# Performance work log

Hardware: AMD Instinct MI355X
Metric: run time of the kernel (lower is better)

## Reference

```python
import jax, jax.numpy as jnp
import numpy as np

B, N, D = 256, 196, 1024   # batch, regions, vis_embed_dim
HID, ATT, SIN, WID, ISD = 1024, 256, 1024, 1024, 256
S = 10                      # sentence steps


def _lin(key, out_dim, in_dim):
    kw, kb = jax.random.split(key)
    w = jax.random.normal(kw, (out_dim, in_dim), jnp.float32) * 0.02
    b = jax.random.normal(kb, (out_dim,), jnp.float32) * 0.02
    return w, b


def setup_inputs() -> dict:
    key = jax.random.key(0)
    ks = jax.random.split(key, 16)
    inp = {}
    inp['vis_enc'] = jax.random.normal(ks[0], (B, N, D), jnp.float32)
    inp['sentences'] = jax.random.randint(ks[1], (B, S, 50), 0, 10000, jnp.int64)
    inp['enc_att_w'], inp['enc_att_b'] = _lin(ks[2], ATT, D)
    inp['dec_att_w'], inp['dec_att_b'] = _lin(ks[3], ATT, HID)
    inp['full_att_w'], inp['full_att_b'] = _lin(ks[4], 1, ATT)
    inp['ctx_w'], inp['ctx_b'] = _lin(ks[5], SIN, D)
    inp['W_ih'], inp['b_ih'] = _lin(ks[6], 4 * HID, SIN)
    inp['W_hh'], inp['b_hh'] = _lin(ks[7], 4 * HID, HID)
    inp['topic_hid_w'], inp['topic_hid_b'] = _lin(ks[8], WID, HID)
    inp['topic_ctx_w'], inp['topic_ctx_b'] = _lin(ks[9], WID, SIN)
    inp['stop_prev_w'], inp['stop_prev_b'] = _lin(ks[10], ISD, HID)
    inp['stop_cur_w'], inp['stop_cur_b'] = _lin(ks[11], ISD, HID)
    inp['final_stop_w'], inp['final_stop_b'] = _lin(ks[12], 2, ISD)
    return inp


def reference(vis_enc, sentences,
              enc_att_w, enc_att_b, dec_att_w, dec_att_b, full_att_w, full_att_b,
              ctx_w, ctx_b, W_ih, b_ih, W_hh, b_hh,
              topic_hid_w, topic_hid_b, topic_ctx_w, topic_ctx_b,
              stop_prev_w, stop_prev_b, stop_cur_w, stop_cur_b,
              final_stop_w, final_stop_b):
    batch, hid = vis_enc.shape[0], W_hh.shape[1]
    sent_num = sentences.shape[1]
    # encoder projection is h-independent -> hoist out of the recurrence
    vis_enc_att = jnp.einsum('bnd,ad->bna', vis_enc, enc_att_w) + enc_att_b  # [B,N,ATT]

    def step(carry, _):
        h, c = carry
        # CoAtt additive attention
        dec = h @ dec_att_w.T + dec_att_b                       # [B,ATT]
        join = jnp.tanh(vis_enc_att + dec[:, None, :])          # [B,N,ATT]
        logits = jnp.einsum('bna,a->bn', join, full_att_w[0]) + full_att_b[0]
        scores = jax.nn.softmax(logits, axis=1)                 # [B,N]
        att_out = jnp.einsum('bn,bnd->bd', scores, vis_enc)     # [B,D]
        ctx = att_out @ ctx_w.T + ctx_b                         # [B,SIN]
        h_prev = h
        # LSTMCell
        gates = ctx @ W_ih.T + b_ih + h @ W_hh.T + b_hh         # [B,4H]
        i, f, g, o = jnp.split(gates, 4, axis=1)
        c_new = jax.nn.sigmoid(f) * c + jax.nn.sigmoid(i) * jnp.tanh(g)
        h_new = jax.nn.sigmoid(o) * jnp.tanh(c_new)
        # topic + stop heads
        topic = jnp.tanh(h_new @ topic_hid_w.T + topic_hid_b
                         + ctx @ topic_ctx_w.T + topic_ctx_b)   # [B,WID]
        p = jnp.tanh(h_prev @ stop_prev_w.T + stop_prev_b
                     + h_new @ stop_cur_w.T + stop_cur_b)
        p = p @ final_stop_w.T + final_stop_b                   # [B,2]
        return (h_new, c_new), (topic, p)

    h0 = jnp.zeros((batch, hid), vis_enc.dtype)
    c0 = jnp.zeros((batch, hid), vis_enc.dtype)
    _, (topics, ps) = jax.lax.scan(step, (h0, c0), None, length=sent_num)
    topics = jnp.transpose(topics, (1, 0, 2))  # [B,S,WID]
    ps = jnp.transpose(ps, (1, 0, 2))          # [B,S,2]
    return topics, ps
```

## Files before the change

kernel.cpp:

```cpp
#include <hip/hip_runtime.h>
#include <hip/hip_bf16.h>
#include <math.h>

static constexpr int BB = 256;
static constexpr int NR = 196;
static constexpr int DV = 1024;
static constexpr int HH = 1024;
static constexpr int AT = 256;
static constexpr int SI = 1024;
static constexpr int WI = 1024;
static constexpr int IS = 256;
static constexpr int ST = 10;

__device__ __forceinline__ float sigmoidf_(float x) { return 1.0f / (1.0f + expf(-x)); }

__device__ __forceinline__ ushort f2bf(float x) {
    uint u = __float_as_uint(x);
    return (ushort)((u + 0x7FFFu + ((u >> 16) & 1u)) >> 16);
}
__device__ __forceinline__ float bf2f(ushort b) { return __uint_as_float(((uint)b) << 16); }

using bf16x8 = __attribute__((ext_vector_type(8))) short;
using f32x4  = __attribute__((ext_vector_type(4))) float;
#define MFMA_B16(a, b, c) __builtin_amdgcn_mfma_f32_16x16x32_bf16((a), (b), (c), 0, 0, 0)

struct CvtTab { const float* s[8]; ushort* h[8]; ushort* l[8]; };

__global__ __launch_bounds__(256) void setup_all(
    CvtTab tab,
    const float* __restrict__ ctxw, ushort* __restrict__ ctT_h, ushort* __restrict__ ctT_l,
    const float* __restrict__ Wih, const float* __restrict__ Wtc,
    const float* __restrict__ cb,
    const float* __restrict__ bih, const float* __restrict__ btc,
    float* __restrict__ out_ih, float* __restrict__ out_tc,
    const float* __restrict__ vis_src, ushort* __restrict__ vis_dst)
{
    __shared__ float T[32][33];
    const int bid = blockIdx.x;

    if (bid < 11264) {
        const int cum[9] = {0, 256, 4352, 5376, 5632, 5888, 6144, 10240, 11264};
        int seg = 0;
#pragma unroll
        for (int i = 1; i < 8; ++i) if (bid >= cum[i]) seg = i;
        const float* s = tab.s[seg];
        ushort* h = tab.h[seg];
        ushort* l = tab.l[seg];
        const int r = bid - cum[seg];
        int rd = r;
        if (seg == 1) rd = (r & 1023) * 4 + (r >> 10);
        const int src = r * 1024 + threadIdx.x * 4;
        const size_t dst = (size_t)rd * 1024 + threadIdx.x * 4;
        float4 v = *(const float4*)(s + src);
        ushort h0 = f2bf(v.x), h1 = f2bf(v.y), h2 = f2bf(v.z), h3 = f2bf(v.w);
        uint2 hq;
        hq.x = h0 | ((uint)h1 << 16); hq.y = h2 | ((uint)h3 << 16);
        *(uint2*)(h + dst) = hq;
        if (seg != 5) {
            uint2 lq;
            ushort l0 = f2bf(v.x - bf2f(h0)), l1 = f2bf(v.y - bf2f(h1));
            ushort l2 = f2bf(v.z - bf2f(h2)), l3 = f2bf(v.w - bf2f(h3));
            lq.x = l0 | ((uint)l1 << 16); lq.y = l2 | ((uint)l3 << 16);
            *(uint2*)(l + dst) = lq;
        }
    } else if (bid < 12288) {
        const int lb = bid - 11264;
        const int tx = threadIdx.x & 31, ty = threadIdx.x >> 5;
        const int k0 = (lb & 31) * 32, n0 = (lb >> 5) * 32;
#pragma unroll
        for (int j = 0; j < 4; ++j)
            T[ty + 8 * j][tx] = ctxw[(size_t)(k0 + ty + 8 * j) * 1024 + n0 + tx];
        __syncthreads();
#pragma unroll
        for (int j = 0; j < 4; ++j) {
            const float v = T[tx][ty + 8 * j];
            const ushort h = f2bf(v);
            const size_t o = (size_t)(n0 + ty + 8 * j) * 1024 + k0 + tx;
            ctT_h[o] = h;
            ctT_l[o] = f2bf(v - bf2f(h));
        }
    } else if (bid < 13568) {
        const int lb = bid - 12288;
        const int lane = threadIdx.x & 63;
        const float* W; const float* b; float* out; int n;
        if (lb < 1024) { W = Wih; b = bih; out = out_ih; n = lb * 4 + (threadIdx.x >> 6); }
        else { W = Wtc; b = btc; out = out_tc; n = (lb - 1024) * 4 + (threadIdx.x >> 6); }
        const float* wr = W + (size_t)n * 1024;
        float p = 0.f;
#pragma unroll
        for (int i = 0; i < 4; ++i) {
            const float4 wv = *(const float4*)&wr[i * 256 + lane * 4];
            const float4 vv = *(const float4*)&cb[i * 256 + lane * 4];
            p = fmaf(wv.x, vv.x, p); p = fmaf(wv.y, vv.y, p);
            p = fmaf(wv.z, vv.z, p); p = fmaf(wv.w, vv.w, p);
        }
        for (int off = 32; off; off >>= 1) p += __shfl_down(p, off);
        if (lane == 0) out[n] = p + b[n];
    } else {
        const int lb = bid - 13568;
        const size_t i = ((size_t)lb * 256 + threadIdx.x) * 8;
        const float4 v0 = *(const float4*)(vis_src + i);
        const float4 v1 = *(const float4*)(vis_src + i + 4);
        uint4 o;
        o.x = f2bf(v0.x) | ((uint)f2bf(v0.y) << 16);
        o.y = f2bf(v0.z) | ((uint)f2bf(v0.w) << 16);
        o.z = f2bf(v1.x) | ((uint)f2bf(v1.y) << 16);
        o.w = f2bf(v1.z) | ((uint)f2bf(v1.w) << 16);
        *(uint4*)(vis_dst + i) = o;
    }
}

__global__ __launch_bounds__(256) void mgemm_wsp2(
    const ushort* __restrict__ A1h, const ushort* __restrict__ A1l,
    ushort* __restrict__ C1h, ushort* __restrict__ C1l,
    const ushort* __restrict__ A2h, const ushort* __restrict__ A2l,
    ushort* __restrict__ C2h, ushort* __restrict__ C2l,
    const ushort* __restrict__ Wh, const ushort* __restrict__ Wl)
{
    __shared__ __align__(16) ushort SM[4 * 64 * 40];
    ushort* Ah = SM; ushort* Al = SM + 2560; ushort* Bh = SM + 5120; ushort* Bl = SM + 7680;

    const int bid = blockIdx.x;
    const int seg1 = (bid < 1024) ? 1 : 0;
    const int lb = seg1 ? bid : (bid - 1024);
    const int bx = lb & 15, by = lb >> 4;
    const int m0 = by * 64, n0 = bx * 64;
    const ushort* Ahg = seg1 ? A1h : A2h;
    const ushort* Alg = seg1 ? A1l : A2l;
    ushort* Ch = seg1 ? C1h : C2h;
    ushort* Cl = seg1 ? C1l : C2l;
    const int N = SI, K = DV;

    const int t = threadIdx.x;
    const int w = t >> 6, lane = t & 63;
    const int l15 = lane & 15, q = lane >> 4;
    const int sr = t >> 2, sq = (t & 3) * 8;
    const int nch = K >> 5;

    f32x4 acc[4] = {};
    uint4 pah, pal, pbh, pbl;
    auto pref = [&](int c) {
        const int k0 = c << 5;
        const size_t ab = (size_t)(m0 + sr) * K + k0 + sq;
        pah = *(const uint4*)&Ahg[ab];
        pal = *(const uint4*)&Alg[ab];
        pbh = *(const uint4*)&Wh[(size_t)(n0 + sr) * K + k0 + sq];
        pbl = *(const uint4*)&Wl[(size_t)(n0 + sr) * K + k0 + sq];
    };
    pref(0);

    for (int c = 0; c < nch; ++c) {
        __syncthreads();
        *(uint4*)&Ah[sr * 40 + sq] = pah;
        *(uint4*)&Al[sr * 40 + sq] = pal;
        *(uint4*)&Bh[sr * 40 + sq] = pbh;
        *(uint4*)&Bl[sr * 40 + sq] = pbl;
        __syncthreads();
        if (c + 1 < nch) pref(c + 1);
        const bf16x8 bh = *(const bf16x8*)&Bh[(w * 16 + l15) * 40 + q * 8];
        const bf16x8 bl = *(const bf16x8*)&Bl[(w * 16 + l15) * 40 + q * 8];
#pragma unroll
        for (int mi = 0; mi < 4; ++mi) {
            const bf16x8 ah = *(const bf16x8*)&Ah[(mi * 16 + l15) * 40 + q * 8];
            const bf16x8 al = *(const bf16x8*)&Al[(mi * 16 + l15) * 40 + q * 8];
            acc[mi] = MFMA_B16(ah, bh, acc[mi]);
            acc[mi] = MFMA_B16(ah, bl, acc[mi]);
            acc[mi] = MFMA_B16(al, bh, acc[mi]);
        }
    }

    const int col = n0 + w * 16 + l15;
#pragma unroll
    for (int mi = 0; mi < 4; ++mi) {
#pragma unroll
        for (int j = 0; j < 4; ++j) {
            const int row = m0 + mi * 16 + q * 4 + j;
            const int ro = seg1 ? ((row & 1023) * 4 + (row >> 10)) : row;
            const float v = acc[mi][j];
            const ushort h = f2bf(v);
            Ch[(size_t)ro * N + col] = h;
            Cl[(size_t)ro * N + col] = f2bf(v - bf2f(h));
        }
    }
}

__global__ __launch_bounds__(256) void mgemm_heads(
    const ushort* __restrict__ tA1h, const ushort* __restrict__ tA1l,
    const ushort* __restrict__ tW1h, const ushort* __restrict__ tW1l,
    const float* __restrict__ tb1,
    const ushort* __restrict__ tA2h, const ushort* __restrict__ tA2l,
    const ushort* __restrict__ tW2h, const ushort* __restrict__ tW2l,
    const float* __restrict__ tb2,
    float* __restrict__ tC,
    const ushort* __restrict__ sA1h, const ushort* __restrict__ sA1l,
    const ushort* __restrict__ sW1h, const ushort* __restrict__ sW1l,
    const float* __restrict__ sb1,
    const ushort* __restrict__ sA2h, const ushort* __restrict__ sA2l,
    const ushort* __restrict__ sW2h, const ushort* __restrict__ sW2l,
    const float* __restrict__ sb2,
    float* __restrict__ sC)
{
    __shared__ __align__(16) ushort SM[4 * 64 * 40];
    ushort* Ah = SM; ushort* Al = SM + 2560; ushort* Bh = SM + 5120; ushort* Bl = SM + 7680;

    const int bid = blockIdx.x;
    const int topic = (bid < 640) ? 1 : 0;
    const int lb = topic ? bid : (bid - 640);
    const int bx = topic ? (lb & 15) : (lb & 3);
    const int by = topic ? (lb >> 4) : (lb >> 2);
    const int m0 = by * 64, n0 = bx * 64;
    const int ldc = topic ? WI : IS;

    const ushort* A1h = topic ? tA1h : sA1h;  const ushort* A1l = topic ? tA1l : sA1l;
    const ushort* W1h = topic ? tW1h : sW1h;  const ushort* W1l = topic ? tW1l : sW1l;
    const float*  b1  = topic ? tb1  : sb1;
    const ushort* A2h = topic ? tA2h : sA2h;  const ushort* A2l = topic ? tA2l : sA2l;
    const ushort* W2h = topic ? tW2h : sW2h;  const ushort* W2l = topic ? tW2l : sW2l;
    const float*  b2  = topic ? tb2  : sb2;
    float* C = topic ? tC : sC;

    const int t = threadIdx.x;
    const int w = t >> 6, lane = t & 63;
    const int l15 = lane & 15, q = lane >> 4;
    const int sr = t >> 2, sq = (t & 3) * 8;
    const int K = HH;
    const int KC = K >> 5, nch = 2 * KC;

    f32x4 acc[4] = {};
    uint4 pah, pal, pbh, pbl;

    auto pref = [&](int c) {
        const int pass = (c >= KC) ? 1 : 0;
        const int k0 = (c - pass * KC) << 5;
        const ushort* Axh = pass ? A2h : A1h;
        const ushort* Axl = pass ? A2l : A1l;
        const ushort* Wh = pass ? W2h : W1h;
        const ushort* Wl = pass ? W2l : W1l;
        const size_t ab = (size_t)(m0 + sr) * K + k0 + sq;
        pah = *(const uint4*)&Axh[ab];
        pal = *(const uint4*)&Axl[ab];
        pbh = *(const uint4*)&Wh[(size_t)(n0 + sr) * K + k0 + sq];
        pbl = *(const uint4*)&Wl[(size_t)(n0 + sr) * K + k0 + sq];
    };
    pref(0);

    for (int c = 0; c < nch; ++c) {
        __syncthreads();
        *(uint4*)&Ah[sr * 40 + sq] = pah;
        *(uint4*)&Al[sr * 40 + sq] = pal;
        *(uint4*)&Bh[sr * 40 + sq] = pbh;
        *(uint4*)&Bl[sr * 40 + sq] = pbl;
        __syncthreads();
        if (c + 1 < nch) pref(c + 1);
        const bf16x8 bh = *(const bf16x8*)&Bh[(w * 16 + l15) * 40 + q * 8];
        const bf16x8 bl = *(const bf16x8*)&Bl[(w * 16 + l15) * 40 + q * 8];
#pragma unroll
        for (int mi = 0; mi < 4; ++mi) {
            const bf16x8 ah = *(const bf16x8*)&Ah[(mi * 16 + l15) * 40 + q * 8];
            const bf16x8 al = *(const bf16x8*)&Al[(mi * 16 + l15) * 40 + q * 8];
            acc[mi] = MFMA_B16(ah, bh, acc[mi]);
            acc[mi] = MFMA_B16(ah, bl, acc[mi]);
            acc[mi] = MFMA_B16(al, bh, acc[mi]);
        }
    }

    const int col = n0 + w * 16 + l15;
    const float bias = b1[col] + b2[col];
#pragma unroll
    for (int mi = 0; mi < 4; ++mi) {
#pragma unroll
        for (int j = 0; j < 4; ++j) {
            const int row = m0 + mi * 16 + q * 4 + j;
            const float v = tanhf(acc[mi][j] + bias);
            if (topic)
                C[((size_t)(row & 255) * ST + (row >> 8)) * ldc + col] = v;
            else
                C[(size_t)row * ldc + col] = v;
        }
    }
}

__global__ __launch_bounds__(512, 6) void mgemm8_lstm(
    const ushort* __restrict__ A1h, const ushort* __restrict__ A1l,
    const ushort* __restrict__ W1h, const ushort* __restrict__ W1l,
    const float* __restrict__ b1,
    const ushort* __restrict__ A2h, const ushort* __restrict__ A2l,
    const ushort* __restrict__ W2h, const ushort* __restrict__ W2l,
    const float* __restrict__ b2,
    int K, float* __restrict__ cvec,
    ushort* __restrict__ hnh, ushort* __restrict__ hnl)
{
    __shared__ __align__(16) ushort SM[26624];

    const int t = threadIdx.x;
    const int m0 = blockIdx.y * 64, n0 = blockIdx.x * 32;
    const int w = t >> 6, lane = t & 63;
    const int g = w >> 2, wg = w & 3;
    const int l15 = lane & 15, q = lane >> 4;
    const int tl = t & 255;
    const int sr = tl >> 2, sq4 = (tl & 3) * 16;
    const int br = tl >> 3, bq = (tl & 7) * 8;
    const int mh = wg >> 1;
    const int colL = (wg & 1) * 16 + l15;

    ushort* Ah = SM + g * 13312;
    ushort* Al = Ah + 4608;
    ushort* Bh = Al + 4608;
    ushort* Bl = Bh + 2048;

    const int nchg = K >> 6;
    const ushort* Ahg = g ? A2h : A1h;
    const ushort* Alg = g ? A2l : A1l;
    const ushort* Wh  = g ? W2h : W1h;
    const ushort* Wl  = g ? W2l : W1l;

    const int bwi = br * 64 + (bq ^ ((br & 7) << 3));

    f32x4 acc[2] = {};
    uint4 pah0, pah1, pal0, pal1, pbh, pbl;
    auto pref = [&](int c) {
        const int k0 = c << 6;
        const size_t ab = (size_t)(m0 + sr) * K + k0 + sq4;
        pah0 = *(const uint4*)&Ahg[ab];
        pah1 = *(const uint4*)&Ahg[ab + 8];
        pal0 = *(const uint4*)&Alg[ab];
        pal1 = *(const uint4*)&Alg[ab + 8];
        pbh = *(const uint4*)&Wh[(size_t)(n0 + br) * K + k0 + bq];
        pbl = *(const uint4*)&Wl[(size_t)(n0 + br) * K + k0 + bq];
    };
    pref(0);

    for (int c = 0; c < nchg; ++c) {
        __syncthreads();
        *(uint4*)&Ah[sr * 72 + sq4]     = pah0;
        *(uint4*)&Ah[sr * 72 + sq4 + 8] = pah1;
        *(uint4*)&Al[sr * 72 + sq4]     = pal0;
        *(uint4*)&Al[sr * 72 + sq4 + 8] = pal1;
        *(uint4*)&Bh[bwi] = pbh;
        *(uint4*)&Bl[bwi] = pbl;
        __syncthreads();
        if (c + 1 < nchg) pref(c + 1);
#pragma unroll
        for (int ks = 0; ks < 2; ++ks) {
            const int bro = colL * 64 + ((ks * 32 + q * 8) ^ ((colL & 7) << 3));
            const bf16x8 bh = *(const bf16x8*)&Bh[bro];
            const bf16x8 bl = *(const bf16x8*)&Bl[bro];
#pragma unroll
            for (int i = 0; i < 2; ++i) {
                const int mi = mh * 2 + i;
                const bf16x8 ah = *(const bf16x8*)&Ah[(mi * 16 + l15) * 72 + ks * 32 + q * 8];
                const bf16x8 al = *(const bf16x8*)&Al[(mi * 16 + l15) * 72 + ks * 32 + q * 8];
                acc[i] = MFMA_B16(ah, bh, acc[i]);
                acc[i] = MFMA_B16(ah, bl, acc[i]);
                acc[i] = MFMA_B16(al, bh, acc[i]);
            }
        }
    }

    float* comb = (float*)(SM + 13312);
    __syncthreads();
    if (g == 1) {
#pragma unroll
        for (int i = 0; i < 2; ++i)
#pragma unroll
            for (int j = 0; j < 4; ++j) comb[tl * 9 + i * 4 + j] = acc[i][j];
    }
    __syncthreads();
    if (g == 0) {
#pragma unroll
        for (int i = 0; i < 2; ++i)
#pragma unroll
            for (int j = 0; j < 4; ++j) acc[i][j] += comb[tl * 9 + i * 4 + j];
    }

    float* G = (float*)(SM + 17920);
    if (g == 0) {
        const int colG = n0 + colL;
        const int gate = colG & 3, unit = colG >> 2;
        const float bias = b1[gate * 1024 + unit] + b2[gate * 1024 + unit];
#pragma unroll
        for (int i = 0; i < 2; ++i) {
            const int mi = mh * 2 + i;
#pragma unroll
            for (int j = 0; j < 4; ++j)
                G[(mi * 16 + q * 4 + j) * 40 + colL] = acc[i][j] + bias;
        }
    }
    __syncthreads();
    {
        const int row = t >> 3, ul = t & 7;
        const float4 g4 = *(const float4*)&G[row * 40 + ul * 4];
        const size_t ci = (size_t)(m0 + row) * HH + (n0 >> 2) + ul;
        const float cn = sigmoidf_(g4.y) * cvec[ci] + sigmoidf_(g4.x) * tanhf(g4.z);
        cvec[ci] = cn;
        const float hv = sigmoidf_(g4.w) * tanhf(cn);
        const ushort hhi = f2bf(hv);
        hnh[ci] = hhi;
        hnl[ci] = f2bf(hv - bf2f(hhi));
    }
}

__global__ __launch_bounds__(512) void mgemm_preb(
    const ushort* __restrict__ vh, const ushort* __restrict__ Wh, const ushort* __restrict__ Wl,
    const float* __restrict__ bias, ushort* __restrict__ C)
{
    __shared__ __align__(16) ushort Avh[128 * 40];
    __shared__ __align__(16) ushort Bh[256 * 40];
    __shared__ __align__(16) ushort Bl[256 * 40];

    const int t = threadIdx.x;
    const int m0 = blockIdx.x * 128;
    const int w = t >> 6, lane = t & 63;
    const int rg = w >> 2, cg = w & 3;
    const int l15 = lane & 15, q = lane >> 4;
    const int ar = t >> 2, ac = (t & 3) * 8;
    const int brr = t >> 1, bc = (t & 1) * 16;
    const int K = DV;

    f32x4 acc[4][4] = {};
    uint4 pa, pbh0, pbh1, pbl0, pbl1;
    auto pref = [&](int c) {
        const int k0 = c << 5;
        pa   = *(const uint4*)&vh[(size_t)(m0 + ar) * K + k0 + ac];
        const size_t bb = (size_t)brr * K + k0 + bc;
        pbh0 = *(const uint4*)&Wh[bb];
        pbh1 = *(const uint4*)&Wh[bb + 8];
        pbl0 = *(const uint4*)&Wl[bb];
        pbl1 = *(const uint4*)&Wl[bb + 8];
    };
    pref(0);

    for (int c = 0; c < 32; ++c) {
        __syncthreads();
        *(uint4*)&Avh[ar * 40 + ac] = pa;
        *(uint4*)&Bh[brr * 40 + bc]     = pbh0;
        *(uint4*)&Bh[brr * 40 + bc + 8] = pbh1;
        *(uint4*)&Bl[brr * 40 + bc]     = pbl0;
        *(uint4*)&Bl[brr * 40 + bc + 8] = pbl1;
        __syncthreads();
        if (c + 1 < 32) pref(c + 1);

        bf16x8 ah[4];
#pragma unroll
        for (int mi = 0; mi < 4; ++mi)
            ah[mi] = *(const bf16x8*)&Avh[(rg * 64 + mi * 16 + l15) * 40 + q * 8];
#pragma unroll
        for (int ni = 0; ni < 4; ++ni) {
            const bf16x8 bh = *(const bf16x8*)&Bh[(cg * 64 + ni * 16 + l15) * 40 + q * 8];
            const bf16x8 bl = *(const bf16x8*)&Bl[(cg * 64 + ni * 16 + l15) * 40 + q * 8];
#pragma unroll
            for (int mi = 0; mi < 4; ++mi) {
                acc[mi][ni] = MFMA_B16(ah[mi], bh, acc[mi][ni]);
                acc[mi][ni] = MFMA_B16(ah[mi], bl, acc[mi][ni]);
            }
        }
    }

#pragma unroll
    for (int ni = 0; ni < 4; ++ni) {
        const int col = cg * 64 + ni * 16 + l15;
        const float bb = bias[col];
#pragma unroll
        for (int mi = 0; mi < 4; ++mi)
#pragma unroll
            for (int j = 0; j < 4; ++j) {
                const int row = m0 + rg * 64 + mi * 16 + q * 4 + j;
                C[(size_t)row * AT + col] = f2bf(acc[mi][ni][j] + bb);
            }
    }
}

template <int VBF>
__global__ __launch_bounds__(1024) void att_step(
    const ushort* __restrict__ vis_att,
    const ushort* __restrict__ hch, const ushort* __restrict__ hcl,
    const ushort* __restrict__ dec_wh, const float* __restrict__ dec_b,
    const float* __restrict__ fw, const float* __restrict__ fbp,
    const void* __restrict__ visp,
    ushort* __restrict__ att_h, ushort* __restrict__ att_l)
{
    const int b = blockIdx.x;
    const int t = threadIdx.x;
    const int lane = t & 63;
    const int w = t >> 6;

    __shared__ float hs[HH];
    __shared__ float decs[AT];
    __shared__ float fwv[AT];
    __shared__ float logit[NR + 4];
    __shared__ float sc[NR + 4];
    __shared__ float red[8];
    __shared__ float part[8][DV];

    hs[t] = bf2f(hch[(size_t)b * HH + t]) + bf2f(hcl[(size_t)b * HH + t]);
    if (t < AT) fwv[t] = fw[t];
    __syncthreads();
    const float fb = fbp[0];

#pragma unroll
    for (int j = 0; j < 16; ++j) {
        const int a = w * 16 + j;
        const ushort* wr = dec_wh + (size_t)a * HH;
        float p = 0.f;
#pragma unroll
        for (int i = 0; i < 2; ++i) {
            const uint4 wv = *(const uint4*)&wr[i * 512 + lane * 8];
            const float4 hv0 = *(const float4*)&hs[i * 512 + lane * 8];
            const float4 hv1 = *(const float4*)&hs[i * 512 + lane * 8 + 4];
            p = fmaf(bf2f((ushort)(wv.x & 0xFFFF)), hv0.x, p);
            p = fmaf(bf2f((ushort)(wv.x >> 16)),    hv0.y, p);
            p = fmaf(bf2f((ushort)(wv.y & 0xFFFF)), hv0.z, p);
            p = fmaf(bf2f((ushort)(wv.y >> 16)),    hv0.w, p);
            p = fmaf(bf2f((ushort)(wv.z & 0xFFFF)), hv1.x, p);
            p = fmaf(bf2f((ushort)(wv.z >> 16)),    hv1.y, p);
            p = fmaf(bf2f((ushort)(wv.w & 0xFFFF)), hv1.z, p);
            p = fmaf(bf2f((ushort)(wv.w >> 16)),    hv1.w, p);
        }
        for (int off = 32; off; off >>= 1) p += __shfl_down(p, off);
        if (lane == 0) decs[a] = p + dec_b[a];
    }
    __syncthreads();

    for (int n = w; n < NR; n += 16) {
        const ushort4 v4 = *(const ushort4*)&vis_att[((size_t)b * NR + n) * AT + lane * 4];
        const int a = lane * 4;
        float s = tanhf(bf2f(v4.x) + decs[a]) * fwv[a];
        s = fmaf(tanhf(bf2f(v4.y) + decs[a + 1]), fwv[a + 1], s);
        s = fmaf(tanhf(bf2f(v4.z) + decs[a + 2]), fwv[a + 2], s);
        s = fmaf(tanhf(bf2f(v4.w) + decs[a + 3]), fwv[a + 3], s);
        for (int off = 32; off; off >>= 1) s += __shfl_down(s, off);
        if (lane == 0) logit[n] = s + fb;
    }
    __syncthreads();

    float m = -1e30f, e = 0.f;
    if (t < NR) m = logit[t];
    if (t < 256) {
        for (int off = 32; off; off >>= 1) m = fmaxf(m, __shfl_down(m, off));
        if (lane == 0) red[w] = m;
    }
    __syncthreads();
    m = fmaxf(fmaxf(red[0], red[1]), fmaxf(red[2], red[3]));
    if (t < NR) e = expf(logit[t] - m);
    if (t < 256) {
        float ss = e;
        for (int off = 32; off; off >>= 1) ss += __shfl_down(ss, off);
        if (lane == 0) red[4 + w] = ss;
    }
    __syncthreads();
    const float S = red[4] + red[5] + red[6] + red[7];
    if (t < NR) sc[t] = e / S;
    __syncthreads();

    const int slice = t >> 7;
    const int c8 = (t & 127) * 8;
    const int nbeg = (slice <= 4) ? 25 * slice : 100 + 24 * (slice - 4);
    const int nend = (slice < 4) ? nbeg + 25 : nbeg + 24;
    float a0 = 0.f, a1 = 0.f, a2 = 0.f, a3 = 0.f;
    float a4 = 0.f, a5 = 0.f, a6 = 0.f, a7 = 0.f;
    if (VBF) {
        const ushort* vb = (const ushort*)visp + (size_t)b * NR * DV + c8;
        for (int n = nbeg; n < nend; ++n) {
            const float s = sc[n];
            const uint4 v = *(const uint4*)&vb[(size_t)n * DV];
            a0 = fmaf(s, bf2f((ushort)(v.x & 0xFFFF)), a0);
            a1 = fmaf(s, bf2f((ushort)(v.x >> 16)), a1);
            a2 = fmaf(s, bf2f((ushort)(v.y & 0xFFFF)), a2);
            a3 = fmaf(s, bf2f((ushort)(v.y >> 16)), a3);
            a4 = fmaf(s, bf2f((ushort)(v.z & 0xFFFF)), a4);
            a5 = fmaf(s, bf2f((ushort)(v.z >> 16)), a5);
            a6 = fmaf(s, bf2f((ushort)(v.w & 0xFFFF)), a6);
            a7 = fmaf(s, bf2f((ushort)(v.w >> 16)), a7);
        }
    } else {
        const float* vb = (const float*)visp + (size_t)b * NR * DV + c8;
        for (int n = nbeg; n < nend; ++n) {
            const float s = sc[n];
            const float4 v0 = *(const float4*)&vb[(size_t)n * DV];
            const float4 v1 = *(const float4*)&vb[(size_t)n * DV + 4];
            a0 = fmaf(s, v0.x, a0); a1 = fmaf(s, v0.y, a1);
            a2 = fmaf(s, v0.z, a2); a3 = fmaf(s, v0.w, a3);
            a4 = fmaf(s, v1.x, a4); a5 = fmaf(s, v1.y, a5);
            a6 = fmaf(s, v1.z, a6); a7 = fmaf(s, v1.w, a7);
        }
    }
    float4 av0; av0.x = a0; av0.y = a1; av0.z = a2; av0.w = a3;
    float4 av1; av1.x = a4; av1.y = a5; av1.z = a6; av1.w = a7;
    *(float4*)&part[slice][c8]     = av0;
    *(float4*)&part[slice][c8 + 4] = av1;
    __syncthreads();
    const float v = ((part[0][t] + part[1][t]) + (part[2][t] + part[3][t]))
                  + ((part[4][t] + part[5][t]) + (part[6][t] + part[7][t]));
    const ushort vh16 = f2bf(v);
    att_h[(size_t)b * DV + t] = vh16;
    att_l[(size_t)b * DV + t] = f2bf(v - bf2f(vh16));
}

__global__ __launch_bounds__(256) void stop_final_all(
    const float* __restrict__ pt, const float* __restrict__ fw,
    const float* __restrict__ fb, float* __restrict__ outp)
{
    const int row = blockIdx.x;
    const int s = row >> 8, b = row & 255;
    const int t = threadIdx.x;
    const int lane = t & 63;
    const int w = t >> 6;

    __shared__ float red[16];
    const float v = pt[(size_t)row * IS + t];
    float p0 = v * fw[t];
    float p1 = v * fw[IS + t];
    for (int off = 32; off; off >>= 1) {
        p0 += __shfl_down(p0, off);
        p1 += __shfl_down(p1, off);
    }
    if (lane == 0) { red[w] = p0; red[8 + w] = p1; }
    __syncthreads();
    if (t == 0) {
        outp[((size_t)b * ST + s) * 2 + 0] = red[0] + red[1] + red[2] + red[3] + fb[0];
        outp[((size_t)b * ST + s) * 2 + 1] = red[8] + red[9] + red[10] + red[11] + fb[1];
    }
}

extern "C" void kernel_launch(void* const* d_in, const int* in_sizes, int n_in,
                              void* d_out, int out_size, void* d_ws, size_t ws_size,
                              hipStream_t stream)
{
    const float* vis        = (const float*)d_in[0];
    const float* enc_att_w  = (const float*)d_in[2];
    const float* enc_att_b  = (const float*)d_in[3];
    const float* dec_att_w  = (const float*)d_in[4];
    const float* dec_att_b  = (const float*)d_in[5];
    const float* full_att_w = (const float*)d_in[6];
    const float* full_att_b = (const float*)d_in[7];
    const float* ctx_w      = (const float*)d_in[8];
    const float* ctx_b      = (const float*)d_in[9];
    const float* W_ih       = (const float*)d_in[10];
    const float* b_ih       = (const float*)d_in[11];
    const float* W_hh       = (const float*)d_in[12];
    const float* b_hh       = (const float*)d_in[13];
    const float* topic_hid_w = (const float*)d_in[14];
    const float* topic_hid_b = (const float*)d_in[15];
    const float* topic_ctx_w = (const float*)d_in[16];
    const float* topic_ctx_b = (const float*)d_in[17];
    const float* stop_prev_w = (const float*)d_in[18];
    const float* stop_prev_b = (const float*)d_in[19];
    const float* stop_cur_w  = (const float*)d_in[20];
    const float* stop_cur_b  = (const float*)d_in[21];
    const float* final_stop_w = (const float*)d_in[22];
    const float* final_stop_b = (const float*)d_in[23];

    float* out_topics = (float*)d_out;
    float* out_ps     = (float*)d_out + (size_t)BB * ST * WI;

    char* ws = (char*)d_ws;
    size_t off = 0;
    auto alloc = [&](size_t bytes) -> void* {
        void* p = (void*)(ws + off);
        off += (bytes + 255) & ~(size_t)255;
        return p;
    };
    ushort* vis_att = (ushort*)alloc((size_t)BB * NR * AT * 2);
    const size_t WTOT = (size_t)11264 * 1024;
    ushort* wh = (ushort*)alloc(WTOT * 2);
    ushort* wl = (ushort*)alloc(WTOT * 2);
    ushort* hh_h   = (ushort*)alloc((size_t)(ST + 1) * BB * HH * 2);
    ushort* hh_l   = (ushort*)alloc((size_t)(ST + 1) * BB * HH * 2);
    ushort* att_all_h = (ushort*)alloc((size_t)ST * BB * DV * 2);
    ushort* att_all_l = (ushort*)alloc((size_t)ST * BB * DV * 2);
    float* cbuf    = (float*)alloc((size_t)BB * HH * 4);
    float* pt_all  = (float*)alloc((size_t)ST * BB * IS * 4);
    ushort* ctT_h  = (ushort*)alloc((size_t)SI * DV * 2);
    ushort* ctT_l  = (ushort*)alloc((size_t)SI * DV * 2);
    ushort* cmb_h  = (ushort*)alloc((size_t)4 * HH * SI * 2);
    ushort* cmb_l  = (ushort*)alloc((size_t)4 * HH * SI * 2);
    ushort* tcc_h  = (ushort*)alloc((size_t)WI * SI * 2);
    ushort* tcc_l  = (ushort*)alloc((size_t)WI * SI * 2);
    float* bf_ih   = (float*)alloc((size_t)4 * HH * 4);
    float* bf_tc   = (float*)alloc((size_t)WI * 4);
    if (off > ws_size) return;
    ushort* vis_bf = nullptr;
    {
        const size_t need = (size_t)BB * NR * DV * 2;
        if (off + need <= ws_size) vis_bf = (ushort*)alloc(need);
    }

    const size_t O_ENC = 0;
    const size_t O_HH  = 262144;
    const size_t O_TH  = 4456448;
    const size_t O_SP  = 5505024;
    const size_t O_SC  = 5767168;
    const size_t O_DEC = 6029312;
    const size_t O_IH2 = 6291456;
    const size_t O_TC2 = 10485760;

    CvtTab tab;
    const float* srcs[8] = {enc_att_w, W_hh, topic_hid_w, stop_prev_w, stop_cur_w,
                            dec_att_w, W_ih, topic_ctx_w};
    const size_t offs[8] = {O_ENC, O_HH, O_TH, O_SP, O_SC, O_DEC, O_IH2, O_TC2};
    for (int i = 0; i < 8; ++i) {
        tab.s[i] = srcs[i];
        tab.h[i] = wh + offs[i];
        tab.l[i] = wl + offs[i];
    }

    hipMemsetAsync(hh_h, 0, (size_t)BB * HH * 2, stream);
    hipMemsetAsync(hh_l, 0, (size_t)BB * HH * 2, stream);
    hipMemsetAsync(cbuf, 0, (size_t)BB * HH * 4, stream);

    setup_all<<<38656, 256, 0, stream>>>(
        tab, ctx_w, ctT_h, ctT_l,
        W_ih, topic_ctx_w, ctx_b, b_ih, topic_ctx_b, bf_ih, bf_tc,
        vis, vis_bf);

    mgemm_wsp2<<<1280, 256, 0, stream>>>(
        wh + O_IH2, wl + O_IH2, cmb_h, cmb_l,
        wh + O_TC2, wl + O_TC2, tcc_h, tcc_l,
        ctT_h, ctT_l);

    mgemm_preb<<<(BB * NR) / 128, 512, 0, stream>>>(
        vis_bf, wh + O_ENC, wl + O_ENC, enc_att_b, vis_att);

    for (int s = 0; s < ST; ++s) {
        ushort* hch = hh_h + (size_t)s * BB * HH;
        ushort* hcl = hh_l + (size_t)s * BB * HH;
        ushort* hnh = hh_h + (size_t)(s + 1) * BB * HH;
        ushort* hnl = hh_l + (size_t)(s + 1) * BB * HH;
        ushort* ath = att_all_h + (size_t)s * BB * DV;
        ushort* atl = att_all_l + (size_t)s * BB * DV;
        att_step<1><<<BB, 1024, 0, stream>>>(vis_att, hch, hcl, wh + O_DEC, dec_att_b,
                                             full_att_w, full_att_b, vis_bf,
                                             ath, atl);
        mgemm8_lstm<<<dim3(4 * HH / 32, BB / 64), 512, 0, stream>>>(
            ath, atl, cmb_h, cmb_l, bf_ih,
            hch, hcl, wh + O_HH, wl + O_HH, b_hh,
            SI, cbuf, hnh, hnl);
    }

    mgemm_heads<<<800, 256, 0, stream>>>(
        hh_h + (size_t)BB * HH, hh_l + (size_t)BB * HH,
        wh + O_TH, wl + O_TH, topic_hid_b,
        att_all_h, att_all_l, tcc_h, tcc_l, bf_tc,
        out_topics,
        hh_h, hh_l, wh + O_SP, wl + O_SP, stop_prev_b,
        hh_h + (size_t)BB * HH, hh_l + (size_t)BB * HH,
        wh + O_SC, wl + O_SC, stop_cur_b,
        pt_all);
    stop_final_all<<<ST * BB, 256, 0, stream>>>(pt_all, final_stop_w, final_stop_b, out_ps);
}
```

Measured before the change: 955.0 us.

## Overlap h@W_hh GEMM with attention step via extra blocks in attention kernel

Moves the recurrent h@W_hh gate GEMM out of the LSTM kernel into 64 extra blocks appended to the attention kernel launch, where it runs concurrently with the per-batch attention blocks and writes fp32 partial gates to a new workspace buffer. The LSTM kernel then splits its K dimension across its two warp groups for the ctx@W_ih product only and adds the precomputed gate partials in the epilogue. This shortens the serial critical path of each recurrent step but adds an extra fp32 gate buffer round trip through memory. The attention kernel now also declares a large static shared array, which may lower its occupancy.

```diff
diff --git a/kernel.cpp b/kernel.cpp
--- a/kernel.cpp
+++ b/kernel.cpp
@@ -280,217 +280,88 @@
     }
 }
 
-__global__ __launch_bounds__(512, 6) void mgemm8_lstm(
-    const ushort* __restrict__ A1h, const ushort* __restrict__ A1l,
-    const ushort* __restrict__ W1h, const ushort* __restrict__ W1l,
-    const float* __restrict__ b1,
-    const ushort* __restrict__ A2h, const ushort* __restrict__ A2l,
-    const ushort* __restrict__ W2h, const ushort* __restrict__ W2l,
-    const float* __restrict__ b2,
-    int K, float* __restrict__ cvec,
-    ushort* __restrict__ hnh, ushort* __restrict__ hnl)
-{
-    __shared__ __align__(16) ushort SM[26624];
-
-    const int t = threadIdx.x;
-    const int m0 = blockIdx.y * 64, n0 = blockIdx.x * 32;
-    const int w = t >> 6, lane = t & 63;
-    const int g = w >> 2, wg = w & 3;
-    const int l15 = lane & 15, q = lane >> 4;
-    const int tl = t & 255;
-    const int sr = tl >> 2, sq4 = (tl & 3) * 16;
-    const int br = tl >> 3, bq = (tl & 7) * 8;
-    const int mh = wg >> 1;
-    const int colL = (wg & 1) * 16 + l15;
-
-    ushort* Ah = SM + g * 13312;
-    ushort* Al = Ah + 4608;
-    ushort* Bh = Al + 4608;
-    ushort* Bl = Bh + 2048;
-
-    const int nchg = K >> 6;
-    const ushort* Ahg = g ? A2h : A1h;
-    const ushort* Alg = g ? A2l : A1l;
-    const ushort* Wh  = g ? W2h : W1h;
-    const ushort* Wl  = g ? W2l : W1l;
-
-    const int bwi = br * 64 + (bq ^ ((br & 7) << 3));
-
-    f32x4 acc[2] = {};
-    uint4 pah0, pah1, pal0, pal1, pbh, pbl;
-    auto pref = [&](int c) {
-        const int k0 = c << 6;
-        const size_t ab = (size_t)(m0 + sr) * K + k0 + sq4;
-        pah0 = *(const uint4*)&Ahg[ab];
-        pah1 = *(const uint4*)&Ahg[ab + 8];
-        pal0 = *(const uint4*)&Alg[ab];
-        pal1 = *(const uint4*)&Alg[ab + 8];
-        pbh = *(const uint4*)&Wh[(size_t)(n0 + br) * K + k0 + bq];
-        pbl = *(const uint4*)&Wl[(size_t)(n0 + br) * K + k0 + bq];
-    };
-    pref(0);
-
-    for (int c = 0; c < nchg; ++c) {
-        __syncthreads();
-        *(uint4*)&Ah[sr * 72 + sq4]     = pah0;
-        *(uint4*)&Ah[sr * 72 + sq4 + 8] = pah1;
-        *(uint4*)&Al[sr * 72 + sq4]     = pal0;
-        *(uint4*)&Al[sr * 72 + sq4 + 8] = pal1;
-        *(uint4*)&Bh[bwi] = pbh;
-        *(uint4*)&Bl[bwi] = pbl;
-        __syncthreads();
-        if (c + 1 < nchg) pref(c + 1);
-#pragma unroll
-        for (int ks = 0; ks < 2; ++ks) {
-            const int bro = colL * 64 + ((ks * 32 + q * 8) ^ ((colL & 7) << 3));
-            const bf16x8 bh = *(const bf16x8*)&Bh[bro];
-            const bf16x8 bl = *(const bf16x8*)&Bl[bro];
-#pragma unroll
-            for (int i = 0; i < 2; ++i) {
-                const int mi = mh * 2 + i;
-                const bf16x8 ah = *(const bf16x8*)&Ah[(mi * 16 + l15) * 72 + ks * 32 + q * 8];
-                const bf16x8 al = *(const bf16x8*)&Al[(mi * 16 + l15) * 72 + ks * 32 + q * 8];
-                acc[i] = MFMA_B16(ah, bh, acc[i]);
-                acc[i] = MFMA_B16(ah, bl, acc[i]);
-                acc[i] = MFMA_B16(al, bh, acc[i]);
-            }
-        }
-    }
-
-    float* comb = (float*)(SM + 13312);
-    __syncthreads();
-    if (g == 1) {
-#pragma unroll
-        for (int i = 0; i < 2; ++i)
-#pragma unroll
-            for (int j = 0; j < 4; ++j) comb[tl * 9 + i * 4 + j] = acc[i][j];
-    }
-    __syncthreads();
-    if (g == 0) {
-#pragma unroll
-        for (int i = 0; i < 2; ++i)
-#pragma unroll
-            for (int j = 0; j < 4; ++j) acc[i][j] += comb[tl * 9 + i * 4 + j];
-    }
-
-    float* G = (float*)(SM + 17920);
-    if (g == 0) {
-        const int colG = n0 + colL;
-        const int gate = colG & 3, unit = colG >> 2;
-        const float bias = b1[gate * 1024 + unit] + b2[gate * 1024 + unit];
-#pragma unroll
-        for (int i = 0; i < 2; ++i) {
-            const int mi = mh * 2 + i;
-#pragma unroll
-            for (int j = 0; j < 4; ++j)
-                G[(mi * 16 + q * 4 + j) * 40 + colL] = acc[i][j] + bias;
-        }
-    }
-    __syncthreads();
-    {
-        const int row = t >> 3, ul = t & 7;
-        const float4 g4 = *(const float4*)&G[row * 40 + ul * 4];
-        const size_t ci = (size_t)(m0 + row) * HH + (n0 >> 2) + ul;
-        const float cn = sigmoidf_(g4.y) * cvec[ci] + sigmoidf_(g4.x) * tanhf(g4.z);
-        cvec[ci] = cn;
-        const float hv = sigmoidf_(g4.w) * tanhf(cn);
-        const ushort hhi = f2bf(hv);
-        hnh[ci] = hhi;
-        hnl[ci] = f2bf(hv - bf2f(hhi));
-    }
-}
-
-__global__ __launch_bounds__(512) void mgemm_preb(
-    const ushort* __restrict__ vh, const ushort* __restrict__ Wh, const ushort* __restrict__ Wl,
-    const float* __restrict__ bias, ushort* __restrict__ C)
-{
-    __shared__ __align__(16) ushort Avh[128 * 40];
-    __shared__ __align__(16) ushort Bh[256 * 40];
-    __shared__ __align__(16) ushort Bl[256 * 40];
-
-    const int t = threadIdx.x;
-    const int m0 = blockIdx.x * 128;
-    const int w = t >> 6, lane = t & 63;
-    const int rg = w >> 2, cg = w & 3;
-    const int l15 = lane & 15, q = lane >> 4;
-    const int ar = t >> 2, ac = (t & 3) * 8;
-    const int brr = t >> 1, bc = (t & 1) * 16;
-    const int K = DV;
-
-    f32x4 acc[4][4] = {};
-    uint4 pa, pbh0, pbh1, pbl0, pbl1;
-    auto pref = [&](int c) {
-        const int k0 = c << 5;
-        pa   = *(const uint4*)&vh[(size_t)(m0 + ar) * K + k0 + ac];
-        const size_t bb = (size_t)brr * K + k0 + bc;
-        pbh0 = *(const uint4*)&Wh[bb];
-        pbh1 = *(const uint4*)&Wh[bb + 8];
-        pbl0 = *(const uint4*)&Wl[bb];
-        pbl1 = *(const uint4*)&Wl[bb + 8];
-    };
-    pref(0);
-
-    for (int c = 0; c < 32; ++c) {
-        __syncthreads();
-        *(uint4*)&Avh[ar * 40 + ac] = pa;
-        *(uint4*)&Bh[brr * 40 + bc]     = pbh0;
-        *(uint4*)&Bh[brr * 40 + bc + 8] = pbh1;
-        *(uint4*)&Bl[brr * 40 + bc]     = pbl0;
-        *(uint4*)&Bl[brr * 40 + bc + 8] = pbl1;
-        __syncthreads();
-        if (c + 1 < 32) pref(c + 1);
-
-        bf16x8 ah[4];
-#pragma unroll
-        for (int mi = 0; mi < 4; ++mi)
-            ah[mi] = *(const bf16x8*)&Avh[(rg * 64 + mi * 16 + l15) * 40 + q * 8];
-#pragma unroll
-        for (int ni = 0; ni < 4; ++ni) {
-            const bf16x8 bh = *(const bf16x8*)&Bh[(cg * 64 + ni * 16 + l15) * 40 + q * 8];
-            const bf16x8 bl = *(const bf16x8*)&Bl[(cg * 64 + ni * 16 + l15) * 40 + q * 8];
-#pragma unroll
-            for (int mi = 0; mi < 4; ++mi) {
-                acc[mi][ni] = MFMA_B16(ah[mi], bh, acc[mi][ni]);
-                acc[mi][ni] = MFMA_B16(ah[mi], bl, acc[mi][ni]);
-            }
-        }
-    }
-
-#pragma unroll
-    for (int ni = 0; ni < 4; ++ni) {
-        const int col = cg * 64 + ni * 16 + l15;
-        const float bb = bias[col];
-#pragma unroll
-        for (int mi = 0; mi < 4; ++mi)
-#pragma unroll
-            for (int j = 0; j < 4; ++j) {
-                const int row = m0 + rg * 64 + mi * 16 + q * 4 + j;
-                C[(size_t)row * AT + col] = f2bf(acc[mi][ni][j] + bb);
-            }
-    }
-}
-
 template <int VBF>
-__global__ __launch_bounds__(1024) void att_step(
+__global__ __launch_bounds__(1024) void att_hgemm(
     const ushort* __restrict__ vis_att,
     const ushort* __restrict__ hch, const ushort* __restrict__ hcl,
     const ushort* __restrict__ dec_wh, const float* __restrict__ dec_b,
     const float* __restrict__ fw, const float* __restrict__ fbp,
     const void* __restrict__ visp,
-    ushort* __restrict__ att_h, ushort* __restrict__ att_l)
+    ushort* __restrict__ att_h, ushort* __restrict__ att_l,
+    const ushort* __restrict__ Whh_h, const ushort* __restrict__ Whh_l,
+    float* __restrict__ Gh)
 {
-    const int b = blockIdx.x;
+    __shared__ __align__(16) char SMRAW[81920];
+    const int bidx = blockIdx.x;
+
+    if (bidx >= BB) {
+        const int lb = bidx - BB;
+        const int sub = threadIdx.x >> 8;
+        const int t = threadIdx.x & 255;
+        ushort* SM = (ushort*)(SMRAW + sub * 20480);
+        ushort* Ah = SM; ushort* Al = SM + 2560;
+        ushort* Bh = SM + 5120; ushort* Bl = SM + 7680;
+        const int tile = lb * 4 + sub;
+        const int m0 = (tile & 3) * 64;
+        const int n0 = (tile >> 2) * 64;
+        const int w = t >> 6, lane = t & 63;
+        const int l15 = lane & 15, q = lane >> 4;
+        const int sr = t >> 2, sq = (t & 3) * 8;
+        const int K = HH, nch = K >> 5;
+
+        f32x4 acc[4] = {};
+        uint4 pah, pal, pbh, pbl;
+        auto pref = [&](int c) {
+            const int k0 = c << 5;
+            const size_t ab = (size_t)(m0 + sr) * K + k0 + sq;
+            pah = *(const uint4*)&hch[ab];
+            pal = *(const uint4*)&hcl[ab];
+            pbh = *(const uint4*)&Whh_h[(size_t)(n0 + sr) * K + k0 + sq];
+            pbl = *(const uint4*)&Whh_l[(size_t)(n0 + sr) * K + k0 + sq];
+        };
+        pref(0);
+
+        for (int c = 0; c < nch; ++c) {
+            __syncthreads();
+            *(uint4*)&Ah[sr * 40 + sq] = pah;
+            *(uint4*)&Al[sr * 40 + sq] = pal;
+            *(uint4*)&Bh[sr * 40 + sq] = pbh;
+            *(uint4*)&Bl[sr * 40 + sq] = pbl;
+            __syncthreads();
+            if (c + 1 < nch) pref(c + 1);
+            const bf16x8 bh = *(const bf16x8*)&Bh[(w * 16 + l15) * 40 + q * 8];
+            const bf16x8 bl = *(const bf16x8*)&Bl[(w * 16 + l15) * 40 + q * 8];
+#pragma unroll
+            for (int mi = 0; mi < 4; ++mi) {
+                const bf16x8 ah = *(const bf16x8*)&Ah[(mi * 16 + l15) * 40 + q * 8];
+                const bf16x8 al = *(const bf16x8*)&Al[(mi * 16 + l15) * 40 + q * 8];
+                acc[mi] = MFMA_B16(ah, bh, acc[mi]);
+                acc[mi] = MFMA_B16(ah, bl, acc[mi]);
+                acc[mi] = MFMA_B16(al, bh, acc[mi]);
+            }
+        }
+
+        const int col = n0 + w * 16 + l15;
+#pragma unroll
+        for (int mi = 0; mi < 4; ++mi)
+#pragma unroll
+            for (int j = 0; j < 4; ++j)
+                Gh[(size_t)(m0 + mi * 16 + q * 4 + j) * 4096 + col] = acc[mi][j];
+        return;
+    }
+
+    float* hs    = (float*)SMRAW;
+    float* decs  = (float*)(SMRAW + 4096);
+    float* fwv   = (float*)(SMRAW + 5120);
+    float* logit = (float*)(SMRAW + 6144);
+    float* sc    = (float*)(SMRAW + 7168);
+    float* red   = (float*)(SMRAW + 8192);
+    float (*part)[DV] = (float(*)[DV])(SMRAW + 8448);
+
+    const int b = bidx;
     const int t = threadIdx.x;
     const int lane = t & 63;
     const int w = t >> 6;
-
-    __shared__ float hs[HH];
-    __shared__ float decs[AT];
-    __shared__ float fwv[AT];
-    __shared__ float logit[NR + 4];
-    __shared__ float sc[NR + 4];
-    __shared__ float red[8];
-    __shared__ float part[8][DV];
 
     hs[t] = bf2f(hch[(size_t)b * HH + t]) + bf2f(hcl[(size_t)b * HH + t]);
     if (t < AT) fwv[t] = fw[t];
@@ -594,6 +465,193 @@
     const ushort vh16 = f2bf(v);
     att_h[(size_t)b * DV + t] = vh16;
     att_l[(size_t)b * DV + t] = f2bf(v - bf2f(vh16));
+}
+
+__global__ __launch_bounds__(512, 6) void mgemm8_lstm(
+    const ushort* __restrict__ A1h, const ushort* __restrict__ A1l,
+    const ushort* __restrict__ W1h, const ushort* __restrict__ W1l,
+    const float* __restrict__ b1, const float* __restrict__ b2,
+    const float* __restrict__ Gh,
+    int K, float* __restrict__ cvec,
+    ushort* __restrict__ hnh, ushort* __restrict__ hnl)
+{
+    __shared__ __align__(16) ushort SM[26624];
+
+    const int t = threadIdx.x;
+    const int m0 = blockIdx.y * 64, n0 = blockIdx.x * 32;
+    const int w = t >> 6, lane = t & 63;
+    const int g = w >> 2, wg = w & 3;
+    const int l15 = lane & 15, q = lane >> 4;
+    const int tl = t & 255;
+    const int sr = tl >> 2, sq4 = (tl & 3) * 16;
+    const int br = tl >> 3, bq = (tl & 7) * 8;
+    const int mh = wg >> 1;
+    const int colL = (wg & 1) * 16 + l15;
+
+    ushort* Ah = SM + g * 13312;
+    ushort* Al = Ah + 4608;
+    ushort* Bh = Al + 4608;
+    ushort* Bl = Bh + 2048;
+
+    const int nchg = K >> 7;
+
+    const int bwi = br * 64 + (bq ^ ((br & 7) << 3));
+
+    f32x4 acc[2] = {};
+    uint4 pah0, pah1, pal0, pal1, pbh, pbl;
+    auto pref = [&](int c) {
+        const int k0 = (c << 6) + (g << 9);
+        const size_t ab = (size_t)(m0 + sr) * K + k0 + sq4;
+        pah0 = *(const uint4*)&A1h[ab];
+        pah1 = *(const uint4*)&A1h[ab + 8];
+        pal0 = *(const uint4*)&A1l[ab];
+        pal1 = *(const uint4*)&A1l[ab + 8];
+        pbh = *(const uint4*)&W1h[(size_t)(n0 + br) * K + k0 + bq];
+        pbl = *(const uint4*)&W1l[(size_t)(n0 + br) * K + k0 + bq];
+    };
+    pref(0);
+
+    for (int c = 0; c < nchg; ++c) {
+        __syncthreads();
+        *(uint4*)&Ah[sr * 72 + sq4]     = pah0;
+        *(uint4*)&Ah[sr * 72 + sq4 + 8] = pah1;
+        *(uint4*)&Al[sr * 72 + sq4]     = pal0;
+        *(uint4*)&Al[sr * 72 + sq4 + 8] = pal1;
+        *(uint4*)&Bh[bwi] = pbh;
+        *(uint4*)&Bl[bwi] = pbl;
+        __syncthreads();
+        if (c + 1 < nchg) pref(c + 1);
+#pragma unroll
+        for (int ks = 0; ks < 2; ++ks) {
+            const int bro = colL * 64 + ((ks * 32 + q * 8) ^ ((colL & 7) << 3));
+            const bf16x8 bh = *(const bf16x8*)&Bh[bro];
+            const bf16x8 bl = *(const bf16x8*)&Bl[bro];
+#pragma unroll
+            for (int i = 0; i < 2; ++i) {
+                const int mi = mh * 2 + i;
+                const bf16x8 ah = *(const bf16x8*)&Ah[(mi * 16 + l15) * 72 + ks * 32 + q * 8];
+                const bf16x8 al = *(const bf16x8*)&Al[(mi * 16 + l15) * 72 + ks * 32 + q * 8];
+                acc[i] = MFMA_B16(ah, bh, acc[i]);
+                acc[i] = MFMA_B16(ah, bl, acc[i]);
+                acc[i] = MFMA_B16(al, bh, acc[i]);
+            }
+        }
+    }
+
+    float* comb = (float*)(SM + 13312);
+    __syncthreads();
+    if (g == 1) {
+#pragma unroll
+        for (int i = 0; i < 2; ++i)
+#pragma unroll
+            for (int j = 0; j < 4; ++j) comb[tl * 9 + i * 4 + j] = acc[i][j];
+    }
+    __syncthreads();
+    if (g == 0) {
+#pragma unroll
+        for (int i = 0; i < 2; ++i)
+#pragma unroll
+            for (int j = 0; j < 4; ++j) acc[i][j] += comb[tl * 9 + i * 4 + j];
+    }
+
+    float* G = (float*)(SM + 17920);
+    if (g == 0) {
+        const int colG = n0 + colL;
+        const int gate = colG & 3, unit = colG >> 2;
+        const float bias = b1[gate * 1024 + unit] + b2[gate * 1024 + unit];
+#pragma unroll
+        for (int i = 0; i < 2; ++i) {
+            const int mi = mh * 2 + i;
+#pragma unroll
+            for (int j = 0; j < 4; ++j) {
+                const int row = mi * 16 + q * 4 + j;
+                G[row * 40 + colL] = acc[i][j] + bias
+                    + Gh[(size_t)(m0 + row) * 4096 + colG];
+            }
+        }
+    }
+    __syncthreads();
+    {
+        const int row = t >> 3, ul = t & 7;
+        const float4 g4 = *(const float4*)&G[row * 40 + ul * 4];
+        const size_t ci = (size_t)(m0 + row) * HH + (n0 >> 2) + ul;
+        const float cn = sigmoidf_(g4.y) * cvec[ci] + sigmoidf_(g4.x) * tanhf(g4.z);
+        cvec[ci] = cn;
+        const float hv = sigmoidf_(g4.w) * tanhf(cn);
+        const ushort hhi = f2bf(hv);
+        hnh[ci] = hhi;
+        hnl[ci] = f2bf(hv - bf2f(hhi));
+    }
+}
+
+__global__ __launch_bounds__(512) void mgemm_preb(
+    const ushort* __restrict__ vh, const ushort* __restrict__ Wh, const ushort* __restrict__ Wl,
+    const float* __restrict__ bias, ushort* __restrict__ C)
+{
+    __shared__ __align__(16) ushort Avh[128 * 40];
+    __shared__ __align__(16) ushort Bh[256 * 40];
+    __shared__ __align__(16) ushort Bl[256 * 40];
+
+    const int t = threadIdx.x;
+    const int m0 = blockIdx.x * 128;
+    const int w = t >> 6, lane = t & 63;
+    const int rg = w >> 2, cg = w & 3;
+    const int l15 = lane & 15, q = lane >> 4;
+    const int ar = t >> 2, ac = (t & 3) * 8;
+    const int brr = t >> 1, bc = (t & 1) * 16;
+    const int K = DV;
+
+    f32x4 acc[4][4] = {};
+    uint4 pa, pbh0, pbh1, pbl0, pbl1;
+    auto pref = [&](int c) {
+        const int k0 = c << 5;
+        pa   = *(const uint4*)&vh[(size_t)(m0 + ar) * K + k0 + ac];
+        const size_t bb = (size_t)brr * K + k0 + bc;
+        pbh0 = *(const uint4*)&Wh[bb];
+        pbh1 = *(const uint4*)&Wh[bb + 8];
+        pbl0 = *(const uint4*)&Wl[bb];
+        pbl1 = *(const uint4*)&Wl[bb + 8];
+    };
+    pref(0);
+
+    for (int c = 0; c < 32; ++c) {
+        __syncthreads();
+        *(uint4*)&Avh[ar * 40 + ac] = pa;
+        *(uint4*)&Bh[brr * 40 + bc]     = pbh0;
+        *(uint4*)&Bh[brr * 40 + bc + 8] = pbh1;
+        *(uint4*)&Bl[brr * 40 + bc]     = pbl0;
+        *(uint4*)&Bl[brr * 40 + bc + 8] = pbl1;
+        __syncthreads();
+        if (c + 1 < 32) pref(c + 1);
+
+        bf16x8 ah[4];
+#pragma unroll
+        for (int mi = 0; mi < 4; ++mi)
+            ah[mi] = *(const bf16x8*)&Avh[(rg * 64 + mi * 16 + l15) * 40 + q * 8];
+#pragma unroll
+        for (int ni = 0; ni < 4; ++ni) {
+            const bf16x8 bh = *(const bf16x8*)&Bh[(cg * 64 + ni * 16 + l15) * 40 + q * 8];
+            const bf16x8 bl = *(const bf16x8*)&Bl[(cg * 64 + ni * 16 + l15) * 40 + q * 8];
+#pragma unroll
+            for (int mi = 0; mi < 4; ++mi) {
+                acc[mi][ni] = MFMA_B16(ah[mi], bh, acc[mi][ni]);
+                acc[mi][ni] = MFMA_B16(ah[mi], bl, acc[mi][ni]);
+            }
+        }
+    }
+
+#pragma unroll
+    for (int ni = 0; ni < 4; ++ni) {
+        const int col = cg * 64 + ni * 16 + l15;
+        const float bb = bias[col];
+#pragma unroll
+        for (int mi = 0; mi < 4; ++mi)
+#pragma unroll
+            for (int j = 0; j < 4; ++j) {
+                const int row = m0 + rg * 64 + mi * 16 + q * 4 + j;
+                C[(size_t)row * AT + col] = f2bf(acc[mi][ni][j] + bb);
+            }
+    }
 }
 
 __global__ __launch_bounds__(256) void stop_final_all(
@@ -670,6 +728,7 @@
     ushort* att_all_l = (ushort*)alloc((size_t)ST * BB * DV * 2);
     float* cbuf    = (float*)alloc((size_t)BB * HH * 4);
     float* pt_all  = (float*)alloc((size_t)ST * BB * IS * 4);
+    float* Gh      = (float*)alloc((size_t)BB * 4 * HH * 4);
     ushort* ctT_h  = (ushort*)alloc((size_t)SI * DV * 2);
     ushort* ctT_l  = (ushort*)alloc((size_t)SI * DV * 2);
     ushort* cmb_h  = (ushort*)alloc((size_t)4 * HH * SI * 2);
@@ -728,12 +787,12 @@
         ushort* hnl = hh_l + (size_t)(s + 1) * BB * HH;
         ushort* ath = att_all_h + (size_t)s * BB * DV;
         ushort* atl = att_all_l + (size_t)s * BB * DV;
-        att_step<1><<<BB, 1024, 0, stream>>>(vis_att, hch, hcl, wh + O_DEC, dec_att_b,
-                                             full_att_w, full_att_b, vis_bf,
-                                             ath, atl);
+        att_hgemm<1><<<BB + 64, 1024, 0, stream>>>(
+            vis_att, hch, hcl, wh + O_DEC, dec_att_b,
+            full_att_w, full_att_b, vis_bf, ath, atl,
+            wh + O_HH, wl + O_HH, Gh);
         mgemm8_lstm<<<dim3(4 * HH / 32, BB / 64), 512, 0, stream>>>(
-            ath, atl, cmb_h, cmb_l, bf_ih,
-            hch, hcl, wh + O_HH, wl + O_HH, b_hh,
+            ath, atl, cmb_h, cmb_l, bf_ih, b_hh, Gh,
             SI, cbuf, hnh, hnl);
     }
 
```

Result: slower. 1.039 ms (+8.8%).
